# Kernel tuning notes

Hardware: AMD Instinct MI355X
Metric: run time of the kernel (lower is better)

Reference implementation:

```python
import jax, jax.numpy as jnp
import numpy as np

NUM_NODES = 1_000_000
EMBED_DIM = 200
NUM_LAYERS = 3   # K
NUM_WALKS = 25   # S
BATCH = 8192


def setup_inputs() -> dict:
    key = jax.random.key(0)
    k_emb, k_ui, k_ii, k_uw, k_iw = jax.random.split(key, 5)
    embeddings = jax.random.normal(k_emb, (NUM_NODES, EMBED_DIM), dtype=jnp.float32) * 0.05
    user_weights = jnp.ones((NUM_LAYERS + 1,), dtype=jnp.float32)
    user_indices = jax.random.randint(k_ui, (BATCH,), 0, NUM_NODES, dtype=jnp.int32)
    item_indices = jax.random.randint(k_ii, (BATCH,), 0, NUM_NODES, dtype=jnp.int32)
    user_walks = jax.random.randint(k_uw, (BATCH, NUM_WALKS, NUM_LAYERS + 1), 0, NUM_NODES, dtype=jnp.int32)
    item_walks = jax.random.randint(k_iw, (BATCH, NUM_WALKS, NUM_LAYERS + 1), 0, NUM_NODES, dtype=jnp.int32)
    return {
        "embeddings": embeddings,
        "user_weights": user_weights,
        "user_indices": user_indices,
        "item_indices": item_indices,
        "user_walks": user_walks,
        "item_walks": item_walks,
    }


def _gwarmer(embeddings, layer_weights, node_indices, walks):
    # embeddings: [N, D]; node_indices: [B]; walks: [B, S, K+1]
    base = embeddings[node_indices]                      # [B, D]   (layer 0)
    gathered = embeddings[walks[:, :, 1:]]               # [B, S, K, D]
    layer_means = gathered.mean(axis=1)                  # [B, K, D] (Eq. 3 mean pool)
    reprs = jnp.concatenate([base[:, None, :], layer_means], axis=1)  # [B, K+1, D]
    w = jax.nn.softmax(layer_weights)                    # self-adaptive weights
    return jnp.einsum('bkd,k->bd', reprs, w)


def reference(embeddings, user_weights, user_indices, item_indices, user_walks, item_walks):
    # NOTE: the original GWarmer.forward uses user_weights for both users and items.
    user_repr = _gwarmer(embeddings, user_weights, user_indices, user_walks)
    item_repr = _gwarmer(embeddings, user_weights, item_indices, item_walks)
    scores = jnp.sum(user_repr * item_repr, axis=1)      # [B] warm inner-product scores
    return scores
```

## Files before the change

### kernel.cpp

```cpp
#include <hip/hip_runtime.h>

#define EMBED_DIM 200
#define NUM_WALKS 25
#define NUM_LAYERS 3
#define BATCH 8192

__global__ __launch_bounds__(256) void gnp_score_kernel(
    const float* __restrict__ emb,
    const float* __restrict__ lw,
    const int*   __restrict__ uidx,
    const int*   __restrict__ iidx,
    const int*   __restrict__ uwalks,
    const int*   __restrict__ iwalks,
    float*       __restrict__ out)
{
    const int lane = threadIdx.x & 63;
    const int b = __builtin_amdgcn_readfirstlane(blockIdx.x * 4 + (threadIdx.x >> 6));

    const float l0 = lw[0], l1 = lw[1], l2 = lw[2], l3 = lw[3];
    const float mx = fmaxf(fmaxf(l0, l1), fmaxf(l2, l3));
    const float e0 = expf(l0 - mx), e1 = expf(l1 - mx);
    const float e2 = expf(l2 - mx), e3 = expf(l3 - mx);
    const float inv = 1.0f / (e0 + e1 + e2 + e3);
    const float w0 = e0 * inv;
    const float c1 = e1 * inv * (1.0f / NUM_WALKS);
    const float c2 = e2 * inv * (1.0f / NUM_WALKS);
    const float c3 = e3 * inv * (1.0f / NUM_WALKS);

    const int dl = (lane < 50) ? lane : 49;
    const unsigned doff = (unsigned)dl * 4u;

    const int* __restrict__ uw = uwalks + b * 100;
    const int* __restrict__ iw = iwalks + b * 100;

    float4 au, ai;
    {
        const unsigned su = (unsigned)uidx[b];
        const unsigned si = (unsigned)iidx[b];
        const float4 uv = *(const float4*)(emb + (size_t)su * 200u + doff);
        const float4 iv = *(const float4*)(emb + (size_t)si * 200u + doff);
        au.x = w0 * uv.x; au.y = w0 * uv.y; au.z = w0 * uv.z; au.w = w0 * uv.w;
        ai.x = w0 * iv.x; ai.y = w0 * iv.y; ai.z = w0 * iv.z; ai.w = w0 * iv.w;
    }

    #pragma unroll
    for (int w = 0; w < NUM_WALKS; ++w) {
        #pragma unroll
        for (int k = 1; k <= NUM_LAYERS; ++k) {
            const float c = (k == 1) ? c1 : (k == 2) ? c2 : c3;
            const unsigned su = (unsigned)uw[w * 4 + k];
            const unsigned si = (unsigned)iw[w * 4 + k];
            const float4 uv = *(const float4*)(emb + (size_t)su * 200u + doff);
            const float4 iv = *(const float4*)(emb + (size_t)si * 200u + doff);
            au.x = fmaf(c, uv.x, au.x); au.y = fmaf(c, uv.y, au.y);
            au.z = fmaf(c, uv.z, au.z); au.w = fmaf(c, uv.w, au.w);
            ai.x = fmaf(c, iv.x, ai.x); ai.y = fmaf(c, iv.y, ai.y);
            ai.z = fmaf(c, iv.z, ai.z); ai.w = fmaf(c, iv.w, ai.w);
        }
    }

    float partial = au.x * ai.x + au.y * ai.y + au.z * ai.z + au.w * ai.w;
    if (lane >= 50) partial = 0.0f;

    #pragma unroll
    for (int off = 32; off > 0; off >>= 1)
        partial += __shfl_xor(partial, off, 64);

    if (lane == 0) out[b] = partial;
}

extern "C" void kernel_launch(void* const* d_in, const int* in_sizes, int n_in,
                              void* d_out, int out_size, void* d_ws, size_t ws_size,
                              hipStream_t stream) {
    const float* emb    = (const float*)d_in[0];
    const float* lw     = (const float*)d_in[1];
    const int*   uidx   = (const int*)d_in[2];
    const int*   iidx   = (const int*)d_in[3];
    const int*   uwalks = (const int*)d_in[4];
    const int*   iwalks = (const int*)d_in[5];
    float*       out    = (float*)d_out;

    const int blocks = BATCH / 4;
    gnp_score_kernel<<<blocks, 256, 0, stream>>>(emb, lw, uidx, iidx,
                                                 uwalks, iwalks, out);
}
```

Measured before the change: 1.020 ms.

## Load walk indices once per wave and broadcast via readlane, roll loop

Each wave now loads its 100 walk indices with one coalesced int2 load per lane and pulls each index out with readlane, instead of issuing scalar loads per walk step. The walk loop is no longer fully unrolled, which shrinks code size and register pressure, and launch bounds now request 4 blocks per CU. Accumulators are split into two chains to shorten FMA dependencies, and row offsets are computed in 32-bit. The rolled loop may expose less memory-level parallelism than the fully unrolled version.

```diff
diff --git a/kernel.cpp b/kernel.cpp
--- a/kernel.cpp
+++ b/kernel.cpp
@@ -5,7 +5,7 @@
 #define NUM_LAYERS 3
 #define BATCH 8192
 
-__global__ __launch_bounds__(256) void gnp_score_kernel(
+__global__ __launch_bounds__(256, 4) void gnp_score_kernel(
     const float* __restrict__ emb,
     const float* __restrict__ lw,
     const int*   __restrict__ uidx,
@@ -30,36 +30,62 @@
     const int dl = (lane < 50) ? lane : 49;
     const unsigned doff = (unsigned)dl * 4u;
 
-    const int* __restrict__ uw = uwalks + b * 100;
-    const int* __restrict__ iw = iwalks + b * 100;
+    const int il2 = (lane < 50) ? lane : 49;
+    const int2 vu = *(const int2*)(uwalks + b * 100 + 2 * il2);
+    const int2 vi = *(const int2*)(iwalks + b * 100 + 2 * il2);
 
-    float4 au, ai;
+    float4 au0, ai0, au1, ai1;
     {
         const unsigned su = (unsigned)uidx[b];
         const unsigned si = (unsigned)iidx[b];
-        const float4 uv = *(const float4*)(emb + (size_t)su * 200u + doff);
-        const float4 iv = *(const float4*)(emb + (size_t)si * 200u + doff);
-        au.x = w0 * uv.x; au.y = w0 * uv.y; au.z = w0 * uv.z; au.w = w0 * uv.w;
-        ai.x = w0 * iv.x; ai.y = w0 * iv.y; ai.z = w0 * iv.z; ai.w = w0 * iv.w;
+        const float4 uv = *(const float4*)(emb + (size_t)(su * 200u) + doff);
+        const float4 iv = *(const float4*)(emb + (size_t)(si * 200u) + doff);
+        au0.x = w0 * uv.x; au0.y = w0 * uv.y; au0.z = w0 * uv.z; au0.w = w0 * uv.w;
+        ai0.x = w0 * iv.x; ai0.y = w0 * iv.y; ai0.z = w0 * iv.z; ai0.w = w0 * iv.w;
+        au1.x = 0.f; au1.y = 0.f; au1.z = 0.f; au1.w = 0.f;
+        ai1.x = 0.f; ai1.y = 0.f; ai1.z = 0.f; ai1.w = 0.f;
     }
 
-    #pragma unroll
     for (int w = 0; w < NUM_WALKS; ++w) {
-        #pragma unroll
-        for (int k = 1; k <= NUM_LAYERS; ++k) {
-            const float c = (k == 1) ? c1 : (k == 2) ? c2 : c3;
-            const unsigned su = (unsigned)uw[w * 4 + k];
-            const unsigned si = (unsigned)iw[w * 4 + k];
-            const float4 uv = *(const float4*)(emb + (size_t)su * 200u + doff);
-            const float4 iv = *(const float4*)(emb + (size_t)si * 200u + doff);
-            au.x = fmaf(c, uv.x, au.x); au.y = fmaf(c, uv.y, au.y);
-            au.z = fmaf(c, uv.z, au.z); au.w = fmaf(c, uv.w, au.w);
-            ai.x = fmaf(c, iv.x, ai.x); ai.y = fmaf(c, iv.y, ai.y);
-            ai.z = fmaf(c, iv.z, ai.z); ai.w = fmaf(c, iv.w, ai.w);
-        }
+        const int j1 = w * 4 + 1;
+        const int j2 = w * 4 + 2;
+        const int j3 = w * 4 + 3;
+        const unsigned su1 = (unsigned)__builtin_amdgcn_readlane(vu.y, j1 >> 1);
+        const unsigned si1 = (unsigned)__builtin_amdgcn_readlane(vi.y, j1 >> 1);
+        const unsigned su2 = (unsigned)__builtin_amdgcn_readlane(vu.x, j2 >> 1);
+        const unsigned si2 = (unsigned)__builtin_amdgcn_readlane(vi.x, j2 >> 1);
+        const unsigned su3 = (unsigned)__builtin_amdgcn_readlane(vu.y, j3 >> 1);
+        const unsigned si3 = (unsigned)__builtin_amdgcn_readlane(vi.y, j3 >> 1);
+
+        const float4 uv1 = *(const float4*)(emb + (size_t)(su1 * 200u) + doff);
+        const float4 iv1 = *(const float4*)(emb + (size_t)(si1 * 200u) + doff);
+        const float4 uv2 = *(const float4*)(emb + (size_t)(su2 * 200u) + doff);
+        const float4 iv2 = *(const float4*)(emb + (size_t)(si2 * 200u) + doff);
+        const float4 uv3 = *(const float4*)(emb + (size_t)(su3 * 200u) + doff);
+        const float4 iv3 = *(const float4*)(emb + (size_t)(si3 * 200u) + doff);
+
+        au0.x = fmaf(c1, uv1.x, au0.x); au0.y = fmaf(c1, uv1.y, au0.y);
+        au0.z = fmaf(c1, uv1.z, au0.z); au0.w = fmaf(c1, uv1.w, au0.w);
+        ai0.x = fmaf(c1, iv1.x, ai0.x); ai0.y = fmaf(c1, iv1.y, ai0.y);
+        ai0.z = fmaf(c1, iv1.z, ai0.z); ai0.w = fmaf(c1, iv1.w, ai0.w);
+
+        au1.x = fmaf(c2, uv2.x, au1.x); au1.y = fmaf(c2, uv2.y, au1.y);
+        au1.z = fmaf(c2, uv2.z, au1.z); au1.w = fmaf(c2, uv2.w, au1.w);
+        ai1.x = fmaf(c2, iv2.x, ai1.x); ai1.y = fmaf(c2, iv2.y, ai1.y);
+        ai1.z = fmaf(c2, iv2.z, ai1.z); ai1.w = fmaf(c2, iv2.w, ai1.w);
+
+        au0.x = fmaf(c3, uv3.x, au0.x); au0.y = fmaf(c3, uv3.y, au0.y);
+        au0.z = fmaf(c3, uv3.z, au0.z); au0.w = fmaf(c3, uv3.w, au0.w);
+        ai0.x = fmaf(c3, iv3.x, ai0.x); ai0.y = fmaf(c3, iv3.y, ai0.y);
+        ai0.z = fmaf(c3, iv3.z, ai0.z); ai0.w = fmaf(c3, iv3.w, ai0.w);
     }
 
-    float partial = au.x * ai.x + au.y * ai.y + au.z * ai.z + au.w * ai.w;
+    const float aux = au0.x + au1.x, auy = au0.y + au1.y;
+    const float auz = au0.z + au1.z, auw = au0.w + au1.w;
+    const float aix = ai0.x + ai1.x, aiy = ai0.y + ai1.y;
+    const float aiz = ai0.z + ai1.z, aiw = ai0.w + ai1.w;
+
+    float partial = aux * aix + auy * aiy + auz * aiz + auw * aiw;
     if (lane >= 50) partial = 0.0f;
 
     #pragma unroll
```

Result: no change. 1.019 ms (-0.1%).
